# Optimization experiments

Hardware: AMD Instinct MI355X
Metric: run time of the kernel (lower is better)

Reference implementation:

```python
import jax, jax.numpy as jnp
import numpy as np

# DeepNovo config constants
MASS_H2O = 18.01056
MASS_NH3 = 17.02655
MS_RESOLUTION = 10.0          # bins per Dalton
WINDOW_SIZE = 10
MAX_MZ = 30000                # 3000 Da * 10 bins/Da
_PAD, _GO, _EOS = 0, 1, 2
VOCAB = 26
BATCH = 32768


def setup_inputs() -> dict:
    key = jax.random.key(0)
    k1, k2, k3, k4 = jax.random.split(key, 4)
    spectrum = jax.random.uniform(k1, (MAX_MZ,), dtype=jnp.float32)
    pepmass = jax.random.uniform(k2, (BATCH,), dtype=jnp.float32, minval=500.0, maxval=2500.0)
    prefix_mass = jax.random.uniform(k3, (BATCH,), dtype=jnp.float32) * pepmass * 0.8
    # amino-acid residue masses roughly in [57, 186] Da
    masses = jax.random.uniform(k4, (VOCAB,), dtype=jnp.float32, minval=57.0, maxval=186.0)
    return {"spectrum": spectrum, "pepmass": pepmass, "prefix_mass": prefix_mass,
            "masses": masses, "direction": 0}


def reference(spectrum, pepmass, prefix_mass, masses, direction):
    if direction == 0:
        first_label, last_label = _GO, _EOS
        cb = prefix_mass[:, None] + masses[None, :]      # [B, V]
        cy = pepmass[:, None] - cb
    else:
        first_label, last_label = _EOS, _GO
        cy = prefix_mass[:, None] + masses[None, :]
        cb = pepmass[:, None] - cy
    # 8 ion types: b, b-H2O, b-NH3, b++, y, y-H2O, y-NH3, y++  -> [B, V, 8]
    ion_mass = jnp.stack([cb, cb - MASS_H2O, cb - MASS_NH3, cb / 2,
                          cy, cy - MASS_H2O, cy - MASS_NH3, cy / 2], axis=-1)
    inf_idx = jnp.round(ion_mass * MS_RESOLUTION).astype(jnp.int32) - WINDOW_SIZE // 2
    valid = (inf_idx >= 0) & (inf_idx <= MAX_MZ - WINDOW_SIZE)   # [B, V, 8]
    safe = jnp.where(valid, inf_idx, 0)
    slices = safe[..., None] + jnp.arange(WINDOW_SIZE, dtype=jnp.int32)  # [B, V, 8, W]
    gathered = jnp.take(spectrum, slices) * valid[..., None].astype(spectrum.dtype)
    # zero out FIRST/LAST/PAD vocab rows (for both directions the set is {_PAD,_GO,_EOS})
    label_mask = jnp.ones((VOCAB,), spectrum.dtype).at[
        jnp.array([_PAD, first_label, last_label])].set(0.0)
    return gathered * label_mask[None, :, None, None]
```

## Files before the change

### kernel.cpp

```cpp
#include <hip/hip_runtime.h>
#include <hip/hip_fp16.h>


#define MASS_H2O 18.01056f
#define MASS_NH3 17.02655f

typedef float floatx4 __attribute__((ext_vector_type(4)));

constexpr int MAX_MZ = 30000;
constexpr int WIN = 10;
constexpr int VOCAB = 26;
constexpr int BLOCK = 640;
constexpr int GRID  = 512;
constexpr int CPB   = VOCAB * 20;
constexpr int MAX_ITERS = 64;

__global__ __launch_bounds__(BLOCK, 5) void intensity_kernel(
    const float* __restrict__ spectrum,
    const float* __restrict__ pepmass,
    const float* __restrict__ prefix_mass,
    const float* __restrict__ masses,
    const int*   __restrict__ dir_p,
    float* __restrict__ out,
    int batch)
{
    __shared__ __half sspec[MAX_MZ];
    __shared__ float  spm[MAX_ITERS];
    __shared__ float  spf[MAX_ITERS];

    const int iters = (batch - (int)blockIdx.x + GRID - 1) / GRID;

    {
        const float2* sp2 = reinterpret_cast<const float2*>(spectrum);
        __half2* dst = reinterpret_cast<__half2*>(sspec);
        for (int i = threadIdx.x; i < MAX_MZ / 2; i += BLOCK) {
            float2 t = sp2[i];
            dst[i] = __floats2half2_rn(t.x, t.y);
        }
    }
    if (threadIdx.x < MAX_ITERS) {
        int k = threadIdx.x;
        int b = (int)blockIdx.x + k * GRID;
        if (k < iters) {
            spm[k] = pepmass[b];
            spf[k] = prefix_mass[b];
        }
    }
    __syncthreads();

    const int c = threadIdx.x;
    if (c >= CPB) return;

    const int dir = dir_p[0];

    const int v = c / 20;
    const int q = c - v * 20;
    const float ms = masses[v];
    const float lmask = (v > 2) ? 1.0f : 0.0f;

    bool  selcy[4];
    float addj[4];
    float mulj[4];
    int   wj[4];
#pragma unroll
    for (int j = 0; j < 4; ++j) {
        int e = 4 * q + j;
        int ion = e / 10;
        wj[j] = e - ion * 10;
        selcy[j] = (ion >= 4);
        int k = ion & 3;
        addj[j] = (k == 1) ? -MASS_H2O : (k == 2) ? -MASS_NH3 : 0.0f;
        mulj[j] = (k == 3) ? 0.5f : 1.0f;
    }

    floatx4* op = reinterpret_cast<floatx4*>(out) + (size_t)blockIdx.x * CPB + c;
    const size_t ostride = (size_t)GRID * CPB;

#pragma unroll 4
    for (int k = 0; k < iters; ++k) {
        float pm = spm[k];
        float pf = spf[k];
        float t = pf + ms;
        float u = pm - t;
        float cb = (dir == 0) ? t : u;
        float cy = (dir == 0) ? u : t;

        float vals[4];
#pragma unroll
        for (int j = 0; j < 4; ++j) {
            float base = selcy[j] ? cy : cb;
            float m = (base + addj[j]) * mulj[j];
            int idx = (int)rintf(m * 10.0f) - (WIN / 2);
            bool valid = (unsigned)idx <= (unsigned)(MAX_MZ - WIN);
            int safe = valid ? idx : 0;
            float s = __half2float(sspec[safe + wj[j]]);
            vals[j] = valid ? s * lmask : 0.0f;
        }

        floatx4 r;
        r.x = vals[0]; r.y = vals[1]; r.z = vals[2]; r.w = vals[3];
        __builtin_nontemporal_store(r, op + (size_t)k * ostride);
    }
}

extern "C" void kernel_launch(void* const* d_in, const int* in_sizes, int n_in,
                              void* d_out, int out_size, void* d_ws, size_t ws_size,
                              hipStream_t stream) {
    const float* spectrum    = (const float*)d_in[0];
    const float* pepmass     = (const float*)d_in[1];
    const float* prefix_mass = (const float*)d_in[2];
    const float* masses      = (const float*)d_in[3];
    const int*   direction   = (const int*)d_in[4];
    float* out = (float*)d_out;

    int batch = in_sizes[1];
    intensity_kernel<<<GRID, BLOCK, 0, stream>>>(
        spectrum, pepmass, prefix_mass, masses, direction, out, batch);
}
```

Before: 293.7 us.

## Drop shared-memory fp16 spectrum staging and gather directly from global memory

```diff
diff --git a/kernel.cpp b/kernel.cpp
--- a/kernel.cpp
+++ b/kernel.cpp
@@ -1,5 +1,4 @@
 #include <hip/hip_runtime.h>
-#include <hip/hip_fp16.h>
 
 
 #define MASS_H2O 18.01056f
@@ -9,13 +8,13 @@
 
 constexpr int MAX_MZ = 30000;
 constexpr int WIN = 10;
-constexpr int VOCAB = 26;
-constexpr int BLOCK = 640;
-constexpr int GRID  = 512;
-constexpr int CPB   = VOCAB * 20;
-constexpr int MAX_ITERS = 64;
+constexpr int CPR = 26 * 20;
+constexpr int BLOCK = 256;
+constexpr int GRID = 2015;
+constexpr int THREADS = GRID * BLOCK;
+constexpr int ROW_STEP = THREADS / CPR;
 
-__global__ __launch_bounds__(BLOCK, 5) void intensity_kernel(
+__global__ __launch_bounds__(BLOCK, 8) void intensity_kernel(
     const float* __restrict__ spectrum,
     const float* __restrict__ pepmass,
     const float* __restrict__ prefix_mass,
@@ -24,62 +23,41 @@
     float* __restrict__ out,
     int batch)
 {
-    __shared__ __half sspec[MAX_MZ];
-    __shared__ float  spm[MAX_ITERS];
-    __shared__ float  spf[MAX_ITERS];
+    const int tid = (int)blockIdx.x * BLOCK + (int)threadIdx.x;
+    const long long total = (long long)batch * CPR;
+    const int n = (int)((total - (long long)tid + (THREADS - 1)) / THREADS);
 
-    const int iters = (batch - (int)blockIdx.x + GRID - 1) / GRID;
-
-    {
-        const float2* sp2 = reinterpret_cast<const float2*>(spectrum);
-        __half2* dst = reinterpret_cast<__half2*>(sspec);
-        for (int i = threadIdx.x; i < MAX_MZ / 2; i += BLOCK) {
-            float2 t = sp2[i];
-            dst[i] = __floats2half2_rn(t.x, t.y);
-        }
-    }
-    if (threadIdx.x < MAX_ITERS) {
-        int k = threadIdx.x;
-        int b = (int)blockIdx.x + k * GRID;
-        if (k < iters) {
-            spm[k] = pepmass[b];
-            spf[k] = prefix_mass[b];
-        }
-    }
-    __syncthreads();
-
-    const int c = threadIdx.x;
-    if (c >= CPB) return;
-
+    const int col  = tid % CPR;
+    const int row0 = tid / CPR;
+    const int v = col / 20;
+    const int q = col - v * 20;
+    const float ms = masses[v];
+    const float lm = (v > 2) ? 1.0f : 0.0f;
     const int dir = dir_p[0];
 
-    const int v = c / 20;
-    const int q = c - v * 20;
-    const float ms = masses[v];
-    const float lmask = (v > 2) ? 1.0f : 0.0f;
-
-    bool  selcy[4];
-    float addj[4];
-    float mulj[4];
+    bool  scy[4];
+    float aj[4];
+    float mj10[4];
     int   wj[4];
 #pragma unroll
     for (int j = 0; j < 4; ++j) {
-        int e = 4 * q + j;
+        int e   = 4 * q + j;
         int ion = e / 10;
-        wj[j] = e - ion * 10;
-        selcy[j] = (ion >= 4);
-        int k = ion & 3;
-        addj[j] = (k == 1) ? -MASS_H2O : (k == 2) ? -MASS_NH3 : 0.0f;
-        mulj[j] = (k == 3) ? 0.5f : 1.0f;
+        wj[j]  = e - ion * 10;
+        scy[j] = (ion >= 4);
+        int kk = ion & 3;
+        aj[j]   = (kk == 1) ? -MASS_H2O : (kk == 2) ? -MASS_NH3 : 0.0f;
+        mj10[j] = (kk == 3) ? 5.0f : 10.0f;
     }
 
-    floatx4* op = reinterpret_cast<floatx4*>(out) + (size_t)blockIdx.x * CPB + c;
-    const size_t ostride = (size_t)GRID * CPB;
+    const float* pm_p = pepmass + row0;
+    const float* pf_p = prefix_mass + row0;
+    floatx4* op = reinterpret_cast<floatx4*>(out) + tid;
 
 #pragma unroll 4
-    for (int k = 0; k < iters; ++k) {
-        float pm = spm[k];
-        float pf = spf[k];
+    for (int k = 0; k < n; ++k) {
+        float pm = pm_p[k * ROW_STEP];
+        float pf = pf_p[k * ROW_STEP];
         float t = pf + ms;
         float u = pm - t;
         float cb = (dir == 0) ? t : u;
@@ -88,18 +66,18 @@
         float vals[4];
 #pragma unroll
         for (int j = 0; j < 4; ++j) {
-            float base = selcy[j] ? cy : cb;
-            float m = (base + addj[j]) * mulj[j];
-            int idx = (int)rintf(m * 10.0f) - (WIN / 2);
+            float base = scy[j] ? cy : cb;
+            float f = (base + aj[j]) * mj10[j];
+            int idx = (int)rintf(f) - (WIN / 2);
             bool valid = (unsigned)idx <= (unsigned)(MAX_MZ - WIN);
-            int safe = valid ? idx : 0;
-            float s = __half2float(sspec[safe + wj[j]]);
-            vals[j] = valid ? s * lmask : 0.0f;
+            int ga = (valid ? idx : 0) + wj[j];
+            float s = spectrum[ga];
+            vals[j] = valid ? s * lm : 0.0f;
         }
 
         floatx4 r;
         r.x = vals[0]; r.y = vals[1]; r.z = vals[2]; r.w = vals[3];
-        __builtin_nontemporal_store(r, op + (size_t)k * ostride);
+        __builtin_nontemporal_store(r, op + (size_t)k * (size_t)THREADS);
     }
 }
 
```

Measured after the change: 341.5 us. +16.3%, slower.
